# Performance work log

Hardware: AMD Instinct MI355X
Metric: run time of the kernel (lower is better)

Reference implementation:

```python
import jax, jax.numpy as jnp
from jax import lax
import numpy as np

INPUT_SIZE = 64
HIDDEN = 16
SEQ_LEN = 512
NUM_CLASSES = 6
BATCH = 1024


def setup_inputs() -> dict:
    key = jax.random.key(0)
    ks = jax.random.split(key, 7)
    s_ih = 1.0 / np.sqrt(HIDDEN)
    return {
        "x": jax.random.normal(ks[0], (BATCH, SEQ_LEN, INPUT_SIZE), dtype=jnp.float32),
        # PyTorch LSTM params: gate order [i, f, g, o]
        "w_ih": jax.random.uniform(ks[1], (4 * HIDDEN, INPUT_SIZE), minval=-s_ih, maxval=s_ih, dtype=jnp.float32),
        "w_hh": jax.random.uniform(ks[2], (4 * HIDDEN, HIDDEN), minval=-s_ih, maxval=s_ih, dtype=jnp.float32),
        "b_ih": jax.random.uniform(ks[3], (4 * HIDDEN,), minval=-s_ih, maxval=s_ih, dtype=jnp.float32),
        "b_hh": jax.random.uniform(ks[4], (4 * HIDDEN,), minval=-s_ih, maxval=s_ih, dtype=jnp.float32),
        "w_fc": jax.random.uniform(ks[5], (NUM_CLASSES, HIDDEN * SEQ_LEN),
                                   minval=-1.0 / np.sqrt(HIDDEN * SEQ_LEN),
                                   maxval=1.0 / np.sqrt(HIDDEN * SEQ_LEN), dtype=jnp.float32),
        "b_fc": jax.random.uniform(ks[6], (NUM_CLASSES,),
                                   minval=-1.0 / np.sqrt(HIDDEN * SEQ_LEN),
                                   maxval=1.0 / np.sqrt(HIDDEN * SEQ_LEN), dtype=jnp.float32),
    }


def reference(x, w_ih, w_hh, b_ih, b_hh, w_fc, b_fc):
    B, T, _ = x.shape
    H = w_hh.shape[1]
    # Precompute input contribution to all gates: [B, T, 4H]
    gates_x = jnp.einsum("bti,gi->btg", x, w_ih) + b_ih + b_hh
    gates_t = jnp.swapaxes(gates_x, 0, 1)  # [T, B, 4H] for scan

    def step(carry, gx):
        h, c = carry
        g = gx + h @ w_hh.T  # [B, 4H]
        i, f, gg, o = jnp.split(g, 4, axis=-1)
        c = jax.nn.sigmoid(f) * c + jax.nn.sigmoid(i) * jnp.tanh(gg)
        h = jax.nn.sigmoid(o) * jnp.tanh(c)
        return (h, c), h

    h0 = jnp.zeros((B, H), x.dtype)
    _, hs = lax.scan(step, (h0, h0), gates_t)  # hs: [T, B, H]
    out = jnp.swapaxes(hs, 0, 1).reshape(B, T * H)  # flatten per batch_first reshape
    return out @ w_fc.T + b_fc
```

## Files before the change

kernel.cpp:

```cpp
#include <hip/hip_runtime.h>
#include <stdint.h>

#define SEQ   512
#define NB    1024
#define NIN   64
#define NH    16
#define NCLS  6
#define GSTRIDE 20
#define GBLK  32
#define NGRP  (SEQ / GBLK)

typedef __attribute__((ext_vector_type(8))) short short8;
typedef __attribute__((ext_vector_type(4))) float f32x4;

#define LOG2E   1.4426950408889634f
#define NK_IFO  (-1.4426950408889634f)
#define NK_G    (-2.8853900817779268f)
#define KC      (-2.8853900817779268f)

#define GKEY(row) (((row) >> 3) & 3)

__device__ __forceinline__ void split8(float4 u0, float4 u1, short8& hi, short8& lo) {
    float f[8] = {u0.x, u0.y, u0.z, u0.w, u1.x, u1.y, u1.z, u1.w};
    #pragma unroll
    for (int j = 0; j < 8; ++j) {
        uint32_t b = __float_as_uint(f[j]);
        uint16_t hb = (uint16_t)(b >> 16);
        hi[j] = (short)hb;
        float hf = __uint_as_float(((uint32_t)hb) << 16);
        lo[j] = (short)(uint16_t)(__float_as_uint(f[j] - hf) >> 16);
    }
}

__device__ __forceinline__ float quad_bcast0(float v) {
    return __int_as_float(__builtin_amdgcn_update_dpp(0, __float_as_int(v), 0x00, 0xF, 0xF, true));
}
__device__ __forceinline__ float quad_bcast1(float v) {
    return __int_as_float(__builtin_amdgcn_update_dpp(0, __float_as_int(v), 0x55, 0xF, 0xF, true));
}
__device__ __forceinline__ float quad_bcast2(float v) {
    return __int_as_float(__builtin_amdgcn_update_dpp(0, __float_as_int(v), 0xAA, 0xF, 0xF, true));
}
__device__ __forceinline__ float quad_bcast3(float v) {
    return __int_as_float(__builtin_amdgcn_update_dpp(0, __float_as_int(v), 0xFF, 0xF, 0xF, true));
}

#define LOAD_TILE(P0, P1, P2, P3, T) do {                       \
    const float* xp_ = xbase + (size_t)(T) * 16 * NIN;          \
    P0 = *(const float4*)(xp_ + 0);                             \
    P1 = *(const float4*)(xp_ + 4);                             \
    P2 = *(const float4*)(xp_ + 32);                            \
    P3 = *(const float4*)(xp_ + 36);                            \
} while (0)

#define COMPUTE_TILE(P0, P1, P2, P3, GB, ROWOFF) do {                          \
    short8 a0h_, a0l_, a1h_, a1l_;                                             \
    split8(P0, P1, a0h_, a0l_);                                                \
    split8(P2, P3, a1h_, a1l_);                                                \
    _Pragma("unroll")                                                          \
    for (int tau = 0; tau < 4; ++tau) {                                        \
        f32x4 c_ = {0.f, 0.f, 0.f, 0.f};                                       \
        c_ = __builtin_amdgcn_mfma_f32_16x16x32_bf16(a0h_, Bh[tau][0], c_, 0, 0, 0); \
        c_ = __builtin_amdgcn_mfma_f32_16x16x32_bf16(a1h_, Bh[tau][1], c_, 0, 0, 0); \
        c_ = __builtin_amdgcn_mfma_f32_16x16x32_bf16(a0l_, Bh[tau][0], c_, 0, 0, 0); \
        c_ = __builtin_amdgcn_mfma_f32_16x16x32_bf16(a0h_, Bl[tau][0], c_, 0, 0, 0); \
        c_ = __builtin_amdgcn_mfma_f32_16x16x32_bf16(a1l_, Bh[tau][1], c_, 0, 0, 0); \
        c_ = __builtin_amdgcn_mfma_f32_16x16x32_bf16(a1h_, Bl[tau][1], c_, 0, 0, 0); \
        f32x4 s_;                                                              \
        s_[0] = fmaf(c_[0], nkt[tau], bwk[tau]);                               \
        s_[1] = fmaf(c_[1], nkt[tau], bwk[tau]);                               \
        s_[2] = fmaf(c_[2], nkt[tau], bwk[tau]);                               \
        s_[3] = fmaf(c_[3], nkt[tau], bwk[tau]);                               \
        *(f32x4*)&(GB)[(ROWOFF) + gidx[tau]] = s_;                             \
    }                                                                          \
} while (0)

__global__ __launch_bounds__(512, 2)
void lstm_ws_kernel(const float* __restrict__ x,
                    const float* __restrict__ w_ih,
                    const float* __restrict__ w_hh,
                    const float* __restrict__ b_ih,
                    const float* __restrict__ b_hh,
                    const float* __restrict__ w_fc,
                    const float* __restrict__ b_fc,
                    float* __restrict__ out)
{
    __shared__ float G [4][2][128 * GSTRIDE];
    __shared__ float HT[4][2][GBLK * NH];

    const int tid  = threadIdx.x;
    const int wid  = tid >> 6;
    const int lane = tid & 63;
    const int e    = wid & 3;
    const int b    = blockIdx.x * 4 + e;
    const bool producer = (wid < 4);

    if (producer) {
        const int ml   = lane & 15;
        const int half = lane >> 4;
        const int kk   = half * 8;

        short8 Bh[4][2], Bl[4][2];
        #pragma unroll
        for (int tau = 0; tau < 4; ++tau) {
            #pragma unroll
            for (int ch = 0; ch < 2; ++ch) {
                const float* wr = w_ih + (tau * 16 + ml) * NIN + ch * 32 + kk;
                float4 u0 = *(const float4*)wr;
                float4 u1 = *(const float4*)(wr + 4);
                split8(u0, u1, Bh[tau][ch], Bl[tau][ch]);
            }
        }
        float nkt[4], bwk[4];
        int   gidx[4];
        #pragma unroll
        for (int tau = 0; tau < 4; ++tau) {
            nkt[tau] = (tau == 2) ? NK_G : NK_IFO;
            bwk[tau] = (b_ih[tau * 16 + ml] + b_hh[tau * 16 + ml]) * nkt[tau];
            const int row = ml * 4 + tau;
            gidx[tau] = row * GSTRIDE + (half ^ GKEY(row)) * 4;
        }

        const float* xbase = x + ((size_t)b * SEQ + ml) * NIN + kk;

        float4 a0, a1, a2, a3;
        float4 b0, b1, b2, b3;

        LOAD_TILE(a0, a1, a2, a3, 0);
        LOAD_TILE(b0, b1, b2, b3, 1);
        COMPUTE_TILE(a0, a1, a2, a3, G[e][0], 0);
        LOAD_TILE(a0, a1, a2, a3, 2);
        COMPUTE_TILE(b0, b1, b2, b3, G[e][0], 64 * GSTRIDE);
        __syncthreads();

        float accfc[NCLS];
        #pragma unroll
        for (int cls = 0; cls < NCLS; ++cls) accfc[cls] = 0.f;

        for (int g = 0; g < NGRP; ++g) {
            if (g < NGRP - 1) {
                LOAD_TILE(b0, b1, b2, b3, 2 * g + 3);
                COMPUTE_TILE(a0, a1, a2, a3, G[e][(g + 1) & 1], 0);
                if (g < NGRP - 2)
                    LOAD_TILE(a0, a1, a2, a3, 2 * g + 4);
                COMPUTE_TILE(b0, b1, b2, b3, G[e][(g + 1) & 1], 64 * GSTRIDE);
            }
            if (g > 0) {
                const int gp = g - 1;
                float4 h4a = *(float4*)&HT[e][gp & 1][lane * 4];
                float4 h4b = *(float4*)&HT[e][gp & 1][256 + lane * 4];
                #pragma unroll
                for (int cls = 0; cls < NCLS; ++cls) {
                    const float* wf = w_fc + cls * (SEQ * NH) + gp * (GBLK * NH);
                    float4 wfa = *(const float4*)(wf + lane * 4);
                    float4 wfb = *(const float4*)(wf + 256 + lane * 4);
                    accfc[cls] = fmaf(h4a.x, wfa.x, accfc[cls]);
                    accfc[cls] = fmaf(h4a.y, wfa.y, accfc[cls]);
                    accfc[cls] = fmaf(h4a.z, wfa.z, accfc[cls]);
                    accfc[cls] = fmaf(h4a.w, wfa.w, accfc[cls]);
                    accfc[cls] = fmaf(h4b.x, wfb.x, accfc[cls]);
                    accfc[cls] = fmaf(h4b.y, wfb.y, accfc[cls]);
                    accfc[cls] = fmaf(h4b.z, wfb.z, accfc[cls]);
                    accfc[cls] = fmaf(h4b.w, wfb.w, accfc[cls]);
                }
            }
            __syncthreads();
        }
        {
            const int gp = NGRP - 1;
            float4 h4a = *(float4*)&HT[e][gp & 1][lane * 4];
            float4 h4b = *(float4*)&HT[e][gp & 1][256 + lane * 4];
            #pragma unroll
            for (int cls = 0; cls < NCLS; ++cls) {
                const float* wf = w_fc + cls * (SEQ * NH) + gp * (GBLK * NH);
                float4 wfa = *(const float4*)(wf + lane * 4);
                float4 wfb = *(const float4*)(wf + 256 + lane * 4);
                accfc[cls] = fmaf(h4a.x, wfa.x, accfc[cls]);
                accfc[cls] = fmaf(h4a.y, wfa.y, accfc[cls]);
                accfc[cls] = fmaf(h4a.z, wfa.z, accfc[cls]);
                accfc[cls] = fmaf(h4a.w, wfa.w, accfc[cls]);
                accfc[cls] = fmaf(h4b.x, wfb.x, accfc[cls]);
                accfc[cls] = fmaf(h4b.y, wfb.y, accfc[cls]);
                accfc[cls] = fmaf(h4b.z, wfb.z, accfc[cls]);
                accfc[cls] = fmaf(h4b.w, wfb.w, accfc[cls]);
            }
        }
        #pragma unroll
        for (int cls = 0; cls < NCLS; ++cls) {
            float v = accfc[cls];
            v += __shfl_xor(v, 1);
            v += __shfl_xor(v, 2);
            v += __shfl_xor(v, 4);
            v += __shfl_xor(v, 8);
            v += __shfl_xor(v, 16);
            v += __shfl_xor(v, 32);
            accfc[cls] = v;
        }
        if (lane == 0) {
            #pragma unroll
            for (int cls = 0; cls < NCLS; ++cls)
                out[b * NCLS + cls] = accfc[cls] + b_fc[cls];
        }
    } else {
        const int gate_t = lane & 3;
        const int u      = lane >> 2;
        const int grow   = gate_t * 16 + u;
        const float nkl  = (gate_t == 2) ? NK_G : NK_IFO;
        float whh[NH];
        #pragma unroll
        for (int j = 0; j < NH; j += 4) {
            float4 w4 = *(const float4*)(w_hh + grow * NH + j);
            whh[j]   = w4.x * nkl;
            whh[j+1] = w4.y * nkl;
            whh[j+2] = w4.z * nkl;
            whh[j+3] = w4.w * nkl;
        }
        const bool  isg = (gate_t == 2);
        const float sO  = isg ? (2.f * KC) : 1.f;
        const float sB  = isg ? (-KC)      : 0.f;

        const int gkey = GKEY(lane);

        int bp_addr[NH];
        #pragma unroll
        for (int j = 0; j < NH; ++j) bp_addr[j] = (4 * j) << 2;

        float C = 0.f;
        float hs[NH];
        #pragma unroll
        for (int j = 0; j < NH; ++j) hs[j] = 0.f;

        __builtin_amdgcn_s_setprio(1);

        __syncthreads();

        for (int g = 0; g < NGRP; ++g) {
            float gvv[GBLK];
            #pragma unroll
            for (int q = 0; q < 8; ++q) {
                f32x4 g4 = *(f32x4*)&G[e][g & 1][(q >> 2) * 64 * GSTRIDE +
                                                 lane * GSTRIDE + (((q & 3) ^ gkey) * 4)];
                gvv[q*4+0] = g4[0]; gvv[q*4+1] = g4[1]; gvv[q*4+2] = g4[2]; gvv[q*4+3] = g4[3];
            }

            float hstore[GBLK];

            #pragma unroll
            for (int r = 0; r < GBLK; ++r) {
                float p0 = fmaf(hs[0],  whh[0],  gvv[r]);
                p0       = fmaf(hs[1],  whh[1],  p0);
                float p1 = hs[2]  * whh[2];   p1 = fmaf(hs[3],  whh[3],  p1);
                float p2 = hs[4]  * whh[4];   p2 = fmaf(hs[5],  whh[5],  p2);
                float p3 = hs[6]  * whh[6];   p3 = fmaf(hs[7],  whh[7],  p3);
                float p4 = hs[8]  * whh[8];   p4 = fmaf(hs[9],  whh[9],  p4);
                float p5 = hs[10] * whh[10];  p5 = fmaf(hs[11], whh[11], p5);
                float p6 = hs[12] * whh[12];  p6 = fmaf(hs[13], whh[13], p6);
                float p7 = hs[14] * whh[14];  p7 = fmaf(hs[15], whh[15], p7);
                const float s01 = p0 + p1, s23 = p2 + p3, s45 = p4 + p5, s67 = p6 + p7;
                const float zp  = (s01 + s23) + (s45 + s67);

                const float ex  = __builtin_amdgcn_exp2f(zp);
                const float act = fmaf(sO, __builtin_amdgcn_rcpf(1.f + ex), sB);

                const float ig = quad_bcast0(act);
                const float fg = quad_bcast1(act);
                const float gg = quad_bcast2(act);
                const float og = quad_bcast3(act);

                const float igg = ig * gg;
                const float t2o = og + og;
                const float nog = -og;

                C = fmaf(fg, C, igg);
                const float e2 = __builtin_amdgcn_exp2f(C);
                const float r2 = __builtin_amdgcn_rcpf(1.f + e2);
                const float hn = fmaf(t2o, r2, nog);

                hstore[r] = hn;

                const int hni = __float_as_int(hn);
                #pragma unroll
                for (int j = 0; j < NH; ++j)
                    hs[j] = __int_as_float(__builtin_amdgcn_ds_bpermute(bp_addr[j], hni));
            }

            if (gate_t == 0) {
                #pragma unroll
                for (int r = 0; r < GBLK; ++r)
                    HT[e][g & 1][r * NH + u] = hstore[r];
            }

            __syncthreads();
        }
    }
}

extern "C" void kernel_launch(void* const* d_in, const int* in_sizes, int n_in,
                              void* d_out, int out_size, void* d_ws, size_t ws_size,
                              hipStream_t stream) {
    const float* x    = (const float*)d_in[0];
    const float* w_ih = (const float*)d_in[1];
    const float* w_hh = (const float*)d_in[2];
    const float* b_ih = (const float*)d_in[3];
    const float* b_hh = (const float*)d_in[4];
    const float* w_fc = (const float*)d_in[5];
    const float* b_fc = (const float*)d_in[6];
    float* out = (float*)d_out;

    hipLaunchKernelGGL(lstm_ws_kernel, dim3(NB / 4), dim3(512), 0, stream,
                       x, w_ih, w_hh, b_ih, b_hh, w_fc, b_fc, out);
}
```

Measured before the change: 224.7 us.

## Pack four batch elements per consumer wave with per-lane full gate computation

Consumer warps previously used one wave per batch element, with 4 lanes per hidden unit (one per gate) exchanging activations through DPP quad broadcasts. Now a single consumer wave handles four batch elements, 16 lanes each, and every lane computes all four gates for its hidden unit. The hidden-state broadcast uses ds_swizzle within 16-lane groups instead of bpermute. This cuts the block from 512 to 320 threads and removes the cross-lane gate exchange, at the cost of four times the per-lane matvec work and more registers. The LDS swizzle key and padding are also adjusted to avoid bank conflicts under the new access pattern.

```diff
diff --git a/kernel.cpp b/kernel.cpp
--- a/kernel.cpp
+++ b/kernel.cpp
@@ -10,6 +10,10 @@
 #define GBLK  32
 #define NGRP  (SEQ / GBLK)
 
+#define GBUF   (128 * GSTRIDE)
+#define GELEM  (2 * GBUF + 8)
+#define HTELEM (2 * GBLK * NH + 8)
+
 typedef __attribute__((ext_vector_type(8))) short short8;
 typedef __attribute__((ext_vector_type(4))) float f32x4;
 
@@ -18,7 +22,7 @@
 #define NK_G    (-2.8853900817779268f)
 #define KC      (-2.8853900817779268f)
 
-#define GKEY(row) (((row) >> 3) & 3)
+#define GKEY2(row) ((((row) >> 3) & 3) ^ (((row) >> 5) & 1))
 
 __device__ __forceinline__ void split8(float4 u0, float4 u1, short8& hi, short8& lo) {
     float f[8] = {u0.x, u0.y, u0.z, u0.w, u1.x, u1.y, u1.z, u1.w};
@@ -30,19 +34,6 @@
         float hf = __uint_as_float(((uint32_t)hb) << 16);
         lo[j] = (short)(uint16_t)(__float_as_uint(f[j] - hf) >> 16);
     }
-}
-
-__device__ __forceinline__ float quad_bcast0(float v) {
-    return __int_as_float(__builtin_amdgcn_update_dpp(0, __float_as_int(v), 0x00, 0xF, 0xF, true));
-}
-__device__ __forceinline__ float quad_bcast1(float v) {
-    return __int_as_float(__builtin_amdgcn_update_dpp(0, __float_as_int(v), 0x55, 0xF, 0xF, true));
-}
-__device__ __forceinline__ float quad_bcast2(float v) {
-    return __int_as_float(__builtin_amdgcn_update_dpp(0, __float_as_int(v), 0xAA, 0xF, 0xF, true));
-}
-__device__ __forceinline__ float quad_bcast3(float v) {
-    return __int_as_float(__builtin_amdgcn_update_dpp(0, __float_as_int(v), 0xFF, 0xF, 0xF, true));
 }
 
 #define LOAD_TILE(P0, P1, P2, P3, T) do {                       \
@@ -75,7 +66,22 @@
     }                                                                          \
 } while (0)
 
-__global__ __launch_bounds__(512, 2)
+#define HSWZ(J) hs[J] = __int_as_float(__builtin_amdgcn_ds_swizzle(hni, (((J) << 5) | 0x10)))
+
+#define MATVEC(T, DST) do {                                                    \
+    float q0 = fmaf(hs[0],  whh[T][0],  gvv[T][r8]);                           \
+    q0       = fmaf(hs[1],  whh[T][1],  q0);                                   \
+    float q1 = hs[2]  * whh[T][2];   q1 = fmaf(hs[3],  whh[T][3],  q1);        \
+    float q2 = hs[4]  * whh[T][4];   q2 = fmaf(hs[5],  whh[T][5],  q2);        \
+    float q3 = hs[6]  * whh[T][6];   q3 = fmaf(hs[7],  whh[T][7],  q3);        \
+    float q4 = hs[8]  * whh[T][8];   q4 = fmaf(hs[9],  whh[T][9],  q4);        \
+    float q5 = hs[10] * whh[T][10];  q5 = fmaf(hs[11], whh[T][11], q5);        \
+    float q6 = hs[12] * whh[T][12];  q6 = fmaf(hs[13], whh[T][13], q6);        \
+    float q7 = hs[14] * whh[T][14];  q7 = fmaf(hs[15], whh[T][15], q7);        \
+    DST = ((q0 + q1) + (q2 + q3)) + ((q4 + q5) + (q6 + q7));                   \
+} while (0)
+
+__global__ __launch_bounds__(320, 2)
 void lstm_ws_kernel(const float* __restrict__ x,
                     const float* __restrict__ w_ih,
                     const float* __restrict__ w_hh,
@@ -85,17 +91,20 @@
                     const float* __restrict__ b_fc,
                     float* __restrict__ out)
 {
-    __shared__ float G [4][2][128 * GSTRIDE];
-    __shared__ float HT[4][2][GBLK * NH];
+    __shared__ float Gf [4 * GELEM];
+    __shared__ float HTf[4 * HTELEM];
 
     const int tid  = threadIdx.x;
     const int wid  = tid >> 6;
     const int lane = tid & 63;
-    const int e    = wid & 3;
-    const int b    = blockIdx.x * 4 + e;
     const bool producer = (wid < 4);
 
     if (producer) {
+        const int e    = wid;
+        const int b    = blockIdx.x * 4 + e;
+        float* Ge  = &Gf [e * GELEM];
+        float* HTe = &HTf[e * HTELEM];
+
         const int ml   = lane & 15;
         const int half = lane >> 4;
         const int kk   = half * 8;
@@ -118,7 +127,7 @@
             nkt[tau] = (tau == 2) ? NK_G : NK_IFO;
             bwk[tau] = (b_ih[tau * 16 + ml] + b_hh[tau * 16 + ml]) * nkt[tau];
             const int row = ml * 4 + tau;
-            gidx[tau] = row * GSTRIDE + (half ^ GKEY(row)) * 4;
+            gidx[tau] = row * GSTRIDE + (half ^ GKEY2(row)) * 4;
         }
 
         const float* xbase = x + ((size_t)b * SEQ + ml) * NIN + kk;
@@ -128,9 +137,9 @@
 
         LOAD_TILE(a0, a1, a2, a3, 0);
         LOAD_TILE(b0, b1, b2, b3, 1);
-        COMPUTE_TILE(a0, a1, a2, a3, G[e][0], 0);
+        COMPUTE_TILE(a0, a1, a2, a3, Ge, 0);
         LOAD_TILE(a0, a1, a2, a3, 2);
-        COMPUTE_TILE(b0, b1, b2, b3, G[e][0], 64 * GSTRIDE);
+        COMPUTE_TILE(b0, b1, b2, b3, Ge, 64 * GSTRIDE);
         __syncthreads();
 
         float accfc[NCLS];
@@ -139,16 +148,18 @@
 
         for (int g = 0; g < NGRP; ++g) {
             if (g < NGRP - 1) {
+                float* Gb = Ge + ((g + 1) & 1) * GBUF;
                 LOAD_TILE(b0, b1, b2, b3, 2 * g + 3);
-                COMPUTE_TILE(a0, a1, a2, a3, G[e][(g + 1) & 1], 0);
+                COMPUTE_TILE(a0, a1, a2, a3, Gb, 0);
                 if (g < NGRP - 2)
                     LOAD_TILE(a0, a1, a2, a3, 2 * g + 4);
-                COMPUTE_TILE(b0, b1, b2, b3, G[e][(g + 1) & 1], 64 * GSTRIDE);
+                COMPUTE_TILE(b0, b1, b2, b3, Gb, 64 * GSTRIDE);
             }
             if (g > 0) {
                 const int gp = g - 1;
-                float4 h4a = *(float4*)&HT[e][gp & 1][lane * 4];
-                float4 h4b = *(float4*)&HT[e][gp & 1][256 + lane * 4];
+                const float* ht = &HTe[(gp & 1) * (GBLK * NH)];
+                float4 h4a = *(const float4*)&ht[lane * 4];
+                float4 h4b = *(const float4*)&ht[256 + lane * 4];
                 #pragma unroll
                 for (int cls = 0; cls < NCLS; ++cls) {
                     const float* wf = w_fc + cls * (SEQ * NH) + gp * (GBLK * NH);
@@ -168,8 +179,9 @@
         }
         {
             const int gp = NGRP - 1;
-            float4 h4a = *(float4*)&HT[e][gp & 1][lane * 4];
-            float4 h4b = *(float4*)&HT[e][gp & 1][256 + lane * 4];
+            const float* ht = &HTe[(gp & 1) * (GBLK * NH)];
+            float4 h4a = *(const float4*)&ht[lane * 4];
+            float4 h4b = *(const float4*)&ht[256 + lane * 4];
             #pragma unroll
             for (int cls = 0; cls < NCLS; ++cls) {
                 const float* wf = w_fc + cls * (SEQ * NH) + gp * (GBLK * NH);
@@ -202,28 +214,29 @@
                 out[b * NCLS + cls] = accfc[cls] + b_fc[cls];
         }
     } else {
-        const int gate_t = lane & 3;
-        const int u      = lane >> 2;
-        const int grow   = gate_t * 16 + u;
-        const float nkl  = (gate_t == 2) ? NK_G : NK_IFO;
-        float whh[NH];
-        #pragma unroll
-        for (int j = 0; j < NH; j += 4) {
-            float4 w4 = *(const float4*)(w_hh + grow * NH + j);
-            whh[j]   = w4.x * nkl;
-            whh[j+1] = w4.y * nkl;
-            whh[j+2] = w4.z * nkl;
-            whh[j+3] = w4.w * nkl;
-        }
-        const bool  isg = (gate_t == 2);
-        const float sO  = isg ? (2.f * KC) : 1.f;
-        const float sB  = isg ? (-KC)      : 0.f;
-
-        const int gkey = GKEY(lane);
-
-        int bp_addr[NH];
-        #pragma unroll
-        for (int j = 0; j < NH; ++j) bp_addr[j] = (4 * j) << 2;
+        const int eq = lane >> 4;
+        const int u  = lane & 15;
+
+        float whh[4][NH];
+        int   rowoff[4], key[4];
+        #pragma unroll
+        for (int t = 0; t < 4; ++t) {
+            const float nk = (t == 2) ? NK_G : NK_IFO;
+            #pragma unroll
+            for (int j = 0; j < NH; j += 4) {
+                float4 w4 = *(const float4*)(w_hh + (t * 16 + u) * NH + j);
+                whh[t][j]   = w4.x * nk;
+                whh[t][j+1] = w4.y * nk;
+                whh[t][j+2] = w4.z * nk;
+                whh[t][j+3] = w4.w * nk;
+            }
+            const int row = u * 4 + t;
+            rowoff[t] = row * GSTRIDE;
+            key[t]    = GKEY2(row);
+        }
+
+        const float* Geq = &Gf [eq * GELEM];
+        float*       HTq = &HTf[eq * HTELEM];
 
         float C = 0.f;
         float hs[NH];
@@ -235,59 +248,57 @@
         __syncthreads();
 
         for (int g = 0; g < NGRP; ++g) {
-            float gvv[GBLK];
-            #pragma unroll
-            for (int q = 0; q < 8; ++q) {
-                f32x4 g4 = *(f32x4*)&G[e][g & 1][(q >> 2) * 64 * GSTRIDE +
-                                                 lane * GSTRIDE + (((q & 3) ^ gkey) * 4)];
-                gvv[q*4+0] = g4[0]; gvv[q*4+1] = g4[1]; gvv[q*4+2] = g4[2]; gvv[q*4+3] = g4[3];
-            }
-
-            float hstore[GBLK];
-
-            #pragma unroll
-            for (int r = 0; r < GBLK; ++r) {
-                float p0 = fmaf(hs[0],  whh[0],  gvv[r]);
-                p0       = fmaf(hs[1],  whh[1],  p0);
-                float p1 = hs[2]  * whh[2];   p1 = fmaf(hs[3],  whh[3],  p1);
-                float p2 = hs[4]  * whh[4];   p2 = fmaf(hs[5],  whh[5],  p2);
-                float p3 = hs[6]  * whh[6];   p3 = fmaf(hs[7],  whh[7],  p3);
-                float p4 = hs[8]  * whh[8];   p4 = fmaf(hs[9],  whh[9],  p4);
-                float p5 = hs[10] * whh[10];  p5 = fmaf(hs[11], whh[11], p5);
-                float p6 = hs[12] * whh[12];  p6 = fmaf(hs[13], whh[13], p6);
-                float p7 = hs[14] * whh[14];  p7 = fmaf(hs[15], whh[15], p7);
-                const float s01 = p0 + p1, s23 = p2 + p3, s45 = p4 + p5, s67 = p6 + p7;
-                const float zp  = (s01 + s23) + (s45 + s67);
-
-                const float ex  = __builtin_amdgcn_exp2f(zp);
-                const float act = fmaf(sO, __builtin_amdgcn_rcpf(1.f + ex), sB);
-
-                const float ig = quad_bcast0(act);
-                const float fg = quad_bcast1(act);
-                const float gg = quad_bcast2(act);
-                const float og = quad_bcast3(act);
-
-                const float igg = ig * gg;
-                const float t2o = og + og;
-                const float nog = -og;
-
-                C = fmaf(fg, C, igg);
-                const float e2 = __builtin_amdgcn_exp2f(C);
-                const float r2 = __builtin_amdgcn_rcpf(1.f + e2);
-                const float hn = fmaf(t2o, r2, nog);
-
-                hstore[r] = hn;
-
-                const int hni = __float_as_int(hn);
+            const float* Gb  = Geq + (g & 1) * GBUF;
+            float*       HTw = HTq + (g & 1) * (GBLK * NH);
+
+            #pragma unroll
+            for (int k = 0; k < 4; ++k) {
+                const int toff = (k >> 1) * (64 * GSTRIDE);
+                const int c0 = (2 * k) & 3, c1 = (2 * k + 1) & 3;
+                float gvv[4][8];
                 #pragma unroll
-                for (int j = 0; j < NH; ++j)
-                    hs[j] = __int_as_float(__builtin_amdgcn_ds_bpermute(bp_addr[j], hni));
-            }
-
-            if (gate_t == 0) {
+                for (int t = 0; t < 4; ++t) {
+                    const float* rp = Gb + toff + rowoff[t];
+                    f32x4 ga = *(const f32x4*)&rp[(c0 ^ key[t]) * 4];
+                    f32x4 gb = *(const f32x4*)&rp[(c1 ^ key[t]) * 4];
+                    gvv[t][0]=ga[0]; gvv[t][1]=ga[1]; gvv[t][2]=ga[2]; gvv[t][3]=ga[3];
+                    gvv[t][4]=gb[0]; gvv[t][5]=gb[1]; gvv[t][6]=gb[2]; gvv[t][7]=gb[3];
+                }
+
                 #pragma unroll
-                for (int r = 0; r < GBLK; ++r)
-                    HT[e][g & 1][r * NH + u] = hstore[r];
+                for (int r8 = 0; r8 < 8; ++r8) {
+                    const int r = k * 8 + r8;
+                    float z0, z1, z2, z3;
+                    MATVEC(0, z0);
+                    MATVEC(1, z1);
+                    MATVEC(2, z2);
+                    MATVEC(3, z3);
+
+                    const float ei = __builtin_amdgcn_exp2f(z0);
+                    const float ef = __builtin_amdgcn_exp2f(z1);
+                    const float eg = __builtin_amdgcn_exp2f(z2);
+                    const float eo = __builtin_amdgcn_exp2f(z3);
+                    const float ai = __builtin_amdgcn_rcpf(1.f + ei);
+                    const float af = __builtin_amdgcn_rcpf(1.f + ef);
+                    const float rg = __builtin_amdgcn_rcpf(1.f + eg);
+                    const float ao = __builtin_amdgcn_rcpf(1.f + eo);
+
+                    const float ag  = fmaf(2.f * KC, rg, -KC);
+                    const float igg = ai * ag;
+                    C = fmaf(af, C, igg);
+
+                    const float e2 = __builtin_amdgcn_exp2f(C);
+                    const float r2 = __builtin_amdgcn_rcpf(1.f + e2);
+                    const float hn = fmaf(ao + ao, r2, -ao);
+
+                    HTw[r * NH + u] = hn;
+
+                    const int hni = __float_as_int(hn);
+                    HSWZ(0);  HSWZ(1);  HSWZ(2);  HSWZ(3);
+                    HSWZ(4);  HSWZ(5);  HSWZ(6);  HSWZ(7);
+                    HSWZ(8);  HSWZ(9);  HSWZ(10); HSWZ(11);
+                    HSWZ(12); HSWZ(13); HSWZ(14); HSWZ(15);
+                }
             }
 
             __syncthreads();
@@ -307,6 +318,6 @@
     const float* b_fc = (const float*)d_in[6];
     float* out = (float*)d_out;
 
-    hipLaunchKernelGGL(lstm_ws_kernel, dim3(NB / 4), dim3(512), 0, stream,
+    hipLaunchKernelGGL(lstm_ws_kernel, dim3(NB / 4), dim3(320), 0, stream,
                        x, w_ih, w_hh, b_ih, b_hh, w_fc, b_fc, out);
 }
```

New measurement: 275.4 us. +22.6%, slower.
